# Optimization experiments

Hardware: AMD Instinct MI355X
Metric: run time of the kernel (lower is better)

## Reference

```python
import jax, jax.numpy as jnp
import numpy as np

DIM = 1024
EXP = 4           # expansion_factor
NUM_EXPERTS = 4
BATCH, SEQ = 4, 4096


def setup_inputs() -> dict:
    key = jax.random.key(0)
    ks = jax.random.split(key, 6)
    x = jax.random.normal(ks[0], (BATCH, SEQ, DIM), dtype=jnp.float32)
    token_mask = jax.random.randint(ks[1], (BATCH, SEQ), 0, NUM_EXPERTS, dtype=jnp.int32)
    hid = DIM * EXP
    s1 = 1.0 / np.sqrt(DIM)
    s2 = 1.0 / np.sqrt(hid)
    # nn.Linear layout: weight [out_features, in_features]
    w1 = jax.random.uniform(ks[2], (hid, DIM), minval=-s1, maxval=s1, dtype=jnp.float32)
    b1 = jax.random.uniform(ks[3], (hid,), minval=-s1, maxval=s1, dtype=jnp.float32)
    w2 = jax.random.uniform(ks[4], (DIM, hid), minval=-s2, maxval=s2, dtype=jnp.float32)
    b2 = jax.random.uniform(ks[5], (DIM,), minval=-s2, maxval=s2, dtype=jnp.float32)
    return {"x": x, "w1": w1, "b1": b1, "w2": w2, "b2": b2, "token_mask": token_mask}


def _nested_ffn(x, w1, b1, w2, b2, token_mask):
    dim = x.shape[-1]            # in_features of proj1
    out_dim = w2.shape[0]        # out_features of proj2 (== dim)
    # Expert m uses the first D_m = width >> (E-1-m) features (matryoshka nesting).
    # Expand (proj1): truncating input features to D_m and doing a full GEMM is
    # exactly equivalent to zeroing features >= D_m, so we mask then do one GEMM.
    d_in = dim >> (NUM_EXPERTS - 1 - token_mask)             # [B,S]
    in_mask = jnp.arange(dim) < d_in[..., None]              # [B,S,dim]
    h = jnp.einsum('bsd,fd->bsf', jnp.where(in_mask, x, jnp.zeros((), x.dtype)), w1) + b1
    h = jax.nn.gelu(h, approximate=False)                    # torch nn.GELU() default = erf
    # Contract (proj2): expert m produces only the first D_m outputs (incl. bias),
    # padded with zeros -> compute full GEMM then mask outputs.
    d_out = out_dim >> (NUM_EXPERTS - 1 - token_mask)        # [B,S]
    out_mask = jnp.arange(out_dim) < d_out[..., None]        # [B,S,out_dim]
    y = jnp.einsum('bsf,df->bsd', h, w2) + b2
    return jnp.where(out_mask, y, jnp.zeros((), y.dtype))


def reference(x, w1, b1, w2, b2, token_mask):
    return _nested_ffn(x, w1, b1, w2, b2, token_mask)
```

## Files before the change

kernel.cpp:

```cpp
#include <hip/hip_runtime.h>
#include <hip/hip_bf16.h>


typedef __bf16 bf16x8 __attribute__((ext_vector_type(8)));
typedef float f32x4 __attribute__((ext_vector_type(4)));

#define M_TOK   16384
#define DIM     1024
#define HID     4096

#define META_TK    40
#define META_BLK   64
#define META_MAP   256
#define META_RT    2560

__device__ inline unsigned int pk_bf16(float a, float b) {
  unsigned int r;
  asm("v_cvt_pk_bf16_f32 %0, %1, %2" : "=v"(r) : "v"(a), "v"(b));
  return r;
}

__device__ inline float gelu_f(float v) {
  float v2 = v * v;
  float w = v * fmaf(0.10294324f, v2, 2.30220830f);
  float e = __builtin_amdgcn_exp2f(-w);
  return v * __builtin_amdgcn_rcpf(1.0f + e);
}

__device__ inline void async_copy16(const void* g, void* s) {
  __builtin_amdgcn_global_load_lds(
      (const __attribute__((address_space(1))) unsigned int*)g,
      (__attribute__((address_space(3))) unsigned int*)s,
      16, 0, 0);
}

template<int ROWS, int LDK>
__device__ inline void stage_tile(const unsigned short* __restrict__ g,
                                  int row0, int k0, char* lds) {
  const char* gbase = (const char*)g;
  int tid = threadIdx.x;
#pragma unroll
  for (int i = 0; i < ROWS / 32; ++i) {
    int q = i * 256 + tid;
    int r = q >> 3;
    int c = q & 7;
    int gc = c ^ (r & 7);
    const void* gp = gbase + ((size_t)(row0 + r) * LDK + (size_t)k0 + gc * 8) * 2;
    async_copy16(gp, lds + (size_t)q * 16);
  }
}

__global__ __launch_bounds__(1024) void sortw_kernel(
    const int* __restrict__ tm,
    const float* __restrict__ w1,
    const float* __restrict__ w2,
    int* __restrict__ meta,
    unsigned short* __restrict__ w1b,
    unsigned short* __restrict__ w2b) {
  int tid = threadIdx.x;
  if (blockIdx.x != 0) {
    size_t i = (size_t)(blockIdx.x - 1) * 4096 + tid * 4;
    const float* src;
    unsigned short* dst;
    if (i < (size_t)HID * DIM) { src = w1; dst = w1b; }
    else { src = w2 - (size_t)HID * DIM; dst = w2b - (size_t)HID * DIM; }
    float4 v = *(const float4*)(src + i);
    uint2 o;
    o.x = pk_bf16(v.x, v.y);
    o.y = pk_bf16(v.z, v.w);
    *(uint2*)(dst + i) = o;
    return;
  }

  __shared__ unsigned short rt[16384];
  __shared__ unsigned int w01[16], w23[16];
  __shared__ int sbase[4];
  __shared__ int cb[128];
  int lane = tid & 63, wv = tid >> 6;

  int c0 = 0, c1 = 0, c2 = 0, c3 = 0;
  unsigned int epack = 0;
  int4 tv[4];
#pragma unroll
  for (int j = 0; j < 4; ++j)
    tv[j] = *(const int4*)(tm + tid * 16 + j * 4);
#pragma unroll
  for (int j = 0; j < 4; ++j) {
    int e;
    e = tv[j].x; epack |= (unsigned)e << (2 * (4 * j + 0)); c0 += (e == 0); c1 += (e == 1); c2 += (e == 2); c3 += (e == 3);
    e = tv[j].y; epack |= (unsigned)e << (2 * (4 * j + 1)); c0 += (e == 0); c1 += (e == 1); c2 += (e == 2); c3 += (e == 3);
    e = tv[j].z; epack |= (unsigned)e << (2 * (4 * j + 2)); c0 += (e == 0); c1 += (e == 1); c2 += (e == 2); c3 += (e == 3);
    e = tv[j].w; epack |= (unsigned)e << (2 * (4 * j + 3)); c0 += (e == 0); c1 += (e == 1); c2 += (e == 2); c3 += (e == 3);
  }
  unsigned int p01 = (unsigned)c0 | ((unsigned)c1 << 16);
  unsigned int p23 = (unsigned)c2 | ((unsigned)c3 << 16);
  unsigned int i01 = p01, i23 = p23;
#pragma unroll
  for (int s = 1; s < 64; s <<= 1) {
    unsigned int t0 = __shfl_up(i01, s, 64);
    unsigned int t1 = __shfl_up(i23, s, 64);
    if (lane >= s) { i01 += t0; i23 += t1; }
  }
  if (lane == 63) { w01[wv] = i01; w23[wv] = i23; }
  unsigned int e01 = i01 - p01, e23 = i23 - p23;
  __syncthreads();
  if (tid < 16) {
    unsigned int a = w01[tid], b = w23[tid];
    unsigned int ia = a, ib = b;
#pragma unroll
    for (int s = 1; s < 16; s <<= 1) {
      unsigned int t0 = __shfl_up(ia, s, 64);
      unsigned int t1 = __shfl_up(ib, s, 64);
      if (tid >= s) { ia += t0; ib += t1; }
    }
    w01[tid] = ia - a;
    w23[tid] = ib - b;
    if (tid == 15) {
      int t0 = (int)(ia & 0xFFFF), t1 = (int)(ia >> 16), t2 = (int)(ib & 0xFFFF);
      sbase[0] = 0; sbase[1] = t0; sbase[2] = t0 + t1; sbase[3] = t0 + t1 + t2;
    }
  }
  __syncthreads();
  int off0 = sbase[0] + (int)((w01[wv] & 0xFFFF) + (e01 & 0xFFFF));
  int off1 = sbase[1] + (int)((w01[wv] >> 16) + (e01 >> 16));
  int off2 = sbase[2] + (int)((w23[wv] & 0xFFFF) + (e23 & 0xFFFF));
  int off3 = sbase[3] + (int)((w23[wv] >> 16) + (e23 >> 16));
#pragma unroll
  for (int j = 0; j < 16; ++j) {
    int e = (epack >> (2 * j)) & 3;
    int t = tid * 16 + j;
    int pos = (e == 0) ? off0++ : (e == 1) ? off1++ : (e == 2) ? off2++ : off3++;
    rt[pos] = (unsigned short)(t | (e << 14));
  }
  __syncthreads();

  if (tid < 128) {
    int last = tid * 128 + 127;
    int e = (last >= sbase[1]) + (last >= sbase[2]) + (last >= sbase[3]);
    cb[tid] = 1 << e;
    meta[META_BLK + tid] = 128 << e;
  }
  __syncthreads();
  if (tid < 8) {
    int k = tid;
    int* map = meta + META_MAP + k * 128;
    int Tk = 0;
    for (int j = 0; j < 16; ++j) Tk += cb[k + 8 * j];
    meta[META_TK + k] = Tk;
    int pos = 0, zpos = Tk;
    for (int j = 0; j < 16; ++j) {
      int s = k + 8 * j;
      int n = cb[s];
      for (int c = 0; c < n; ++c) map[pos++] = s * 8 + c;
      for (int c = n; c < 8; ++c) map[zpos++] = s * 8 + c;
    }
  }
  int* rowtok = meta + META_RT;
#pragma unroll
  for (int j = 0; j < 16; ++j)
    rowtok[j * 1024 + tid] = (int)rt[j * 1024 + tid];
}

__global__ void prepx_kernel(const float* __restrict__ x,
                             const int* __restrict__ meta,
                             unsigned short* __restrict__ xb) {
  int b = blockIdx.x;
  int tid = threadIdx.x;
  int mt = meta[META_RT + b];
  int t = mt & 0x3FFF;
  int din = 128 << (mt >> 14);
  int kb = meta[META_BLK + (b >> 7)];
  int d = tid * 4;
  if (d < kb) {
    uint2 o; o.x = 0; o.y = 0;
    if (d < din) {
      float4 v = *(const float4*)(x + (size_t)t * DIM + d);
      o.x = pk_bf16(v.x, v.y);
      o.y = pk_bf16(v.z, v.w);
    }
    *(uint2*)(xb + (size_t)b * DIM + d) = o;
  }
}

__global__ __launch_bounds__(256) void gemm1_kernel(
    const unsigned short* __restrict__ A,
    const unsigned short* __restrict__ B,
    const float* __restrict__ bias,
    const int* __restrict__ meta,
    unsigned short* __restrict__ H)
{
  constexpr int K = DIM, N = HID;
  __shared__ char smem[32768];
  char* As = smem;
  char* Bs = smem + 16384;
  int tid = threadIdx.x;
  int lane = tid & 63, quad = lane >> 4, l15 = lane & 15;
  int wave = tid >> 6, wm = wave & 1, wn = wave >> 1;
  int rowblk = 127 - (blockIdx.x >> 5);
  int row0 = rowblk * 128, col0 = (blockIdx.x & 31) * 128;
  int kmax = meta[META_BLK + rowblk];

  int chb = (quad ^ (l15 & 7)) << 4;

  f32x4 acc[4][4] = {};

  for (int k0 = 0; k0 < kmax; k0 += 64) {
    __syncthreads();
    stage_tile<128, K>(A, row0, k0, As);
    stage_tile<128, K>(B, col0, k0, Bs);
    __syncthreads();
#pragma unroll
    for (int kk = 0; kk < 2; ++kk) {
      int xo = chb ^ (kk << 6);
      bf16x8 af[4], bg[4];
#pragma unroll
      for (int mt = 0; mt < 4; ++mt)
        af[mt] = *(const bf16x8*)(As + (wm * 64 + mt * 16 + l15) * 128 + xo);
#pragma unroll
      for (int nt = 0; nt < 4; ++nt)
        bg[nt] = *(const bf16x8*)(Bs + (wn * 64 + nt * 16 + l15) * 128 + xo);
#pragma unroll
      for (int mt = 0; mt < 4; ++mt)
#pragma unroll
        for (int nt = 0; nt < 4; ++nt)
          acc[mt][nt] = __builtin_amdgcn_mfma_f32_16x16x32_bf16(
              bg[nt], af[mt], acc[mt][nt], 0, 0, 0);
    }
  }

  int t_base = row0 + wm * 64;
  int f_base = col0 + wn * 64;
#pragma unroll
  for (int nt = 0; nt < 4; ++nt) {
    int f0 = f_base + nt * 16 + quad * 4;
    float4 bv = *(const float4*)(bias + f0);
#pragma unroll
    for (int mt = 0; mt < 4; ++mt) {
      int t = t_base + mt * 16 + l15;
      float v0 = gelu_f(acc[mt][nt][0] + bv.x);
      float v1 = gelu_f(acc[mt][nt][1] + bv.y);
      float v2 = gelu_f(acc[mt][nt][2] + bv.z);
      float v3 = gelu_f(acc[mt][nt][3] + bv.w);
      uint2 p;
      p.x = pk_bf16(v0, v1);
      p.y = pk_bf16(v2, v3);
      *(uint2*)(H + (size_t)t * N + f0) = p;
    }
  }
}

__global__ __launch_bounds__(256) void gemm2_kernel(
    const unsigned short* __restrict__ A,
    const unsigned short* __restrict__ B,
    const float* __restrict__ bias,
    const int* __restrict__ meta,
    float* __restrict__ out)
{
  constexpr int K = HID, N = DIM;
  int Bk = blockIdx.x & 7, ord = blockIdx.x >> 3;
  int Tk = meta[META_TK + Bk];
  int mp = meta[META_MAP + Bk * 128 + ord];
  int row0 = (mp >> 3) * 128, col0 = (mp & 7) * 128;
  const int* rowtok = meta + META_RT;
  int tid = threadIdx.x;

  if (ord >= Tk) {
    float4 z = make_float4(0.f, 0.f, 0.f, 0.f);
#pragma unroll
    for (int i = 0; i < 16; ++i) {
      int idx = i * 256 + tid;
      int r = idx >> 5;
      int col = (idx & 31) * 4;
      int t = rowtok[row0 + r] & 0x3FFF;
      *(float4*)(out + (size_t)t * N + col0 + col) = z;
    }
    return;
  }

  __shared__ char smem[32768];
  char* As = smem;
  char* Bs = smem + 16384;
  int lane = tid & 63, quad = lane >> 4, l15 = lane & 15;
  int wave = tid >> 6, wm = wave & 1, wn = wave >> 1;
  int chb = (quad ^ (l15 & 7)) << 4;

  f32x4 acc[4][4] = {};

  for (int k0 = 0; k0 < K; k0 += 64) {
    __syncthreads();
    stage_tile<128, K>(A, row0, k0, As);
    stage_tile<128, K>(B, col0, k0, Bs);
    __syncthreads();
#pragma unroll
    for (int kk = 0; kk < 2; ++kk) {
      int xo = chb ^ (kk << 6);
      bf16x8 af[4], bg[4];
#pragma unroll
      for (int mt = 0; mt < 4; ++mt)
        af[mt] = *(const bf16x8*)(As + (wm * 64 + mt * 16 + l15) * 128 + xo);
#pragma unroll
      for (int nt = 0; nt < 4; ++nt)
        bg[nt] = *(const bf16x8*)(Bs + (wn * 64 + nt * 16 + l15) * 128 + xo);
#pragma unroll
      for (int mt = 0; mt < 4; ++mt)
#pragma unroll
        for (int nt = 0; nt < 4; ++nt)
          acc[mt][nt] = __builtin_amdgcn_mfma_f32_16x16x32_bf16(
              bg[nt], af[mt], acc[mt][nt], 0, 0, 0);
    }
  }

  int p_base = row0 + wm * 64;
  int d_base = col0 + wn * 64;
  float4 bv[4];
#pragma unroll
  for (int nt = 0; nt < 4; ++nt)
    bv[nt] = *(const float4*)(bias + d_base + nt * 16 + quad * 4);
#pragma unroll
  for (int mt = 0; mt < 4; ++mt) {
    int m2 = rowtok[p_base + mt * 16 + l15];
    int t = m2 & 0x3FFF;
    int dout = 128 << (m2 >> 14);
#pragma unroll
    for (int nt = 0; nt < 4; ++nt) {
      int d0 = d_base + nt * 16 + quad * 4;
      bool ok = d0 < dout;
      float4 o;
      o.x = ok ? acc[mt][nt][0] + bv[nt].x : 0.0f;
      o.y = ok ? acc[mt][nt][1] + bv[nt].y : 0.0f;
      o.z = ok ? acc[mt][nt][2] + bv[nt].z : 0.0f;
      o.w = ok ? acc[mt][nt][3] + bv[nt].w : 0.0f;
      *(float4*)(out + (size_t)t * N + d0) = o;
    }
  }
}

extern "C" void kernel_launch(void* const* d_in, const int* in_sizes, int n_in,
                              void* d_out, int out_size, void* d_ws, size_t ws_size,
                              hipStream_t stream) {
  const float* x  = (const float*)d_in[0];
  const float* w1 = (const float*)d_in[1];
  const float* b1 = (const float*)d_in[2];
  const float* w2 = (const float*)d_in[3];
  const float* b2 = (const float*)d_in[4];
  const int*   tm = (const int*)d_in[5];
  float* out = (float*)d_out;

  char* ws = (char*)d_ws;
  int* meta = (int*)ws;
  unsigned short* xb  = (unsigned short*)(ws + 131072);
  unsigned short* w1b = (unsigned short*)(ws + 33685504);
  unsigned short* w2b = (unsigned short*)(ws + 42074112);
  unsigned short* hb  = (unsigned short*)(ws + 50462720);

  sortw_kernel<<<2049, 1024, 0, stream>>>(tm, w1, w2, meta, w1b, w2b);
  prepx_kernel<<<M_TOK, 256, 0, stream>>>(x, meta, xb);
  gemm1_kernel<<<4096, 256, 0, stream>>>(xb, w1b, b1, meta, hb);
  gemm2_kernel<<<1024, 256, 0, stream>>>(hb, w2b, b2, meta, out);
}
```

Baseline: 324.9 us.

## Double-buffer LDS tiles in both GEMM kernels to overlap loads with MFMA

Both GEMM kernels now use two 32KB LDS buffers. The next k-tile is staged into the alternate buffer while MFMAs consume the current one, and the loop uses one barrier per iteration instead of two. The aim is to hide global-to-LDS latency behind compute. The cost is that LDS per block doubles to 64KB, which reduces how many blocks can be resident per CU.

```diff
diff --git a/kernel.cpp b/kernel.cpp
--- a/kernel.cpp
+++ b/kernel.cpp
@@ -190,9 +190,7 @@
     unsigned short* __restrict__ H)
 {
   constexpr int K = DIM, N = HID;
-  __shared__ char smem[32768];
-  char* As = smem;
-  char* Bs = smem + 16384;
+  __shared__ char smem[65536];
   int tid = threadIdx.x;
   int lane = tid & 63, quad = lane >> 4, l15 = lane & 15;
   int wave = tid >> 6, wm = wave & 1, wn = wave >> 1;
@@ -204,11 +202,21 @@
 
   f32x4 acc[4][4] = {};
 
-  for (int k0 = 0; k0 < kmax; k0 += 64) {
-    __syncthreads();
-    stage_tile<128, K>(A, row0, k0, As);
-    stage_tile<128, K>(B, col0, k0, Bs);
-    __syncthreads();
+  stage_tile<128, K>(A, row0, 0, smem);
+  stage_tile<128, K>(B, col0, 0, smem + 16384);
+  __syncthreads();
+
+  int nt = kmax >> 6;
+  for (int t = 0; t < nt; ++t) {
+    char* buf = smem + ((t & 1) << 15);
+    if (t + 1 < nt) {
+      char* nbuf = smem + (((t + 1) & 1) << 15);
+      int kn = (t + 1) << 6;
+      stage_tile<128, K>(A, row0, kn, nbuf);
+      stage_tile<128, K>(B, col0, kn, nbuf + 16384);
+    }
+    char* As = buf;
+    char* Bs = buf + 16384;
 #pragma unroll
     for (int kk = 0; kk < 2; ++kk) {
       int xo = chb ^ (kk << 6);
@@ -217,30 +225,31 @@
       for (int mt = 0; mt < 4; ++mt)
         af[mt] = *(const bf16x8*)(As + (wm * 64 + mt * 16 + l15) * 128 + xo);
 #pragma unroll
-      for (int nt = 0; nt < 4; ++nt)
-        bg[nt] = *(const bf16x8*)(Bs + (wn * 64 + nt * 16 + l15) * 128 + xo);
+      for (int nt2 = 0; nt2 < 4; ++nt2)
+        bg[nt2] = *(const bf16x8*)(Bs + (wn * 64 + nt2 * 16 + l15) * 128 + xo);
 #pragma unroll
       for (int mt = 0; mt < 4; ++mt)
 #pragma unroll
-        for (int nt = 0; nt < 4; ++nt)
-          acc[mt][nt] = __builtin_amdgcn_mfma_f32_16x16x32_bf16(
-              bg[nt], af[mt], acc[mt][nt], 0, 0, 0);
-    }
+        for (int nt2 = 0; nt2 < 4; ++nt2)
+          acc[mt][nt2] = __builtin_amdgcn_mfma_f32_16x16x32_bf16(
+              bg[nt2], af[mt], acc[mt][nt2], 0, 0, 0);
+    }
+    __syncthreads();
   }
 
   int t_base = row0 + wm * 64;
   int f_base = col0 + wn * 64;
 #pragma unroll
-  for (int nt = 0; nt < 4; ++nt) {
-    int f0 = f_base + nt * 16 + quad * 4;
+  for (int nt2 = 0; nt2 < 4; ++nt2) {
+    int f0 = f_base + nt2 * 16 + quad * 4;
     float4 bv = *(const float4*)(bias + f0);
 #pragma unroll
     for (int mt = 0; mt < 4; ++mt) {
       int t = t_base + mt * 16 + l15;
-      float v0 = gelu_f(acc[mt][nt][0] + bv.x);
-      float v1 = gelu_f(acc[mt][nt][1] + bv.y);
-      float v2 = gelu_f(acc[mt][nt][2] + bv.z);
-      float v3 = gelu_f(acc[mt][nt][3] + bv.w);
+      float v0 = gelu_f(acc[mt][nt2][0] + bv.x);
+      float v1 = gelu_f(acc[mt][nt2][1] + bv.y);
+      float v2 = gelu_f(acc[mt][nt2][2] + bv.z);
+      float v3 = gelu_f(acc[mt][nt2][3] + bv.w);
       uint2 p;
       p.x = pk_bf16(v0, v1);
       p.y = pk_bf16(v2, v3);
@@ -277,20 +286,28 @@
     return;
   }
 
-  __shared__ char smem[32768];
-  char* As = smem;
-  char* Bs = smem + 16384;
+  __shared__ char smem[65536];
   int lane = tid & 63, quad = lane >> 4, l15 = lane & 15;
   int wave = tid >> 6, wm = wave & 1, wn = wave >> 1;
   int chb = (quad ^ (l15 & 7)) << 4;
 
   f32x4 acc[4][4] = {};
 
-  for (int k0 = 0; k0 < K; k0 += 64) {
-    __syncthreads();
-    stage_tile<128, K>(A, row0, k0, As);
-    stage_tile<128, K>(B, col0, k0, Bs);
-    __syncthreads();
+  stage_tile<128, K>(A, row0, 0, smem);
+  stage_tile<128, K>(B, col0, 0, smem + 16384);
+  __syncthreads();
+
+  constexpr int NT = K >> 6;
+  for (int t = 0; t < NT; ++t) {
+    char* buf = smem + ((t & 1) << 15);
+    if (t + 1 < NT) {
+      char* nbuf = smem + (((t + 1) & 1) << 15);
+      int kn = (t + 1) << 6;
+      stage_tile<128, K>(A, row0, kn, nbuf);
+      stage_tile<128, K>(B, col0, kn, nbuf + 16384);
+    }
+    char* As = buf;
+    char* Bs = buf + 16384;
 #pragma unroll
     for (int kk = 0; kk < 2; ++kk) {
       int xo = chb ^ (kk << 6);
@@ -299,37 +316,38 @@
       for (int mt = 0; mt < 4; ++mt)
         af[mt] = *(const bf16x8*)(As + (wm * 64 + mt * 16 + l15) * 128 + xo);
 #pragma unroll
-      for (int nt = 0; nt < 4; ++nt)
-        bg[nt] = *(const bf16x8*)(Bs + (wn * 64 + nt * 16 + l15) * 128 + xo);
+      for (int nt2 = 0; nt2 < 4; ++nt2)
+        bg[nt2] = *(const bf16x8*)(Bs + (wn * 64 + nt2 * 16 + l15) * 128 + xo);
 #pragma unroll
       for (int mt = 0; mt < 4; ++mt)
 #pragma unroll
-        for (int nt = 0; nt < 4; ++nt)
-          acc[mt][nt] = __builtin_amdgcn_mfma_f32_16x16x32_bf16(
-              bg[nt], af[mt], acc[mt][nt], 0, 0, 0);
-    }
+        for (int nt2 = 0; nt2 < 4; ++nt2)
+          acc[mt][nt2] = __builtin_amdgcn_mfma_f32_16x16x32_bf16(
+              bg[nt2], af[mt], acc[mt][nt2], 0, 0, 0);
+    }
+    __syncthreads();
   }
 
   int p_base = row0 + wm * 64;
   int d_base = col0 + wn * 64;
   float4 bv[4];
 #pragma unroll
-  for (int nt = 0; nt < 4; ++nt)
-    bv[nt] = *(const float4*)(bias + d_base + nt * 16 + quad * 4);
+  for (int nt2 = 0; nt2 < 4; ++nt2)
+    bv[nt2] = *(const float4*)(bias + d_base + nt2 * 16 + quad * 4);
 #pragma unroll
   for (int mt = 0; mt < 4; ++mt) {
     int m2 = rowtok[p_base + mt * 16 + l15];
     int t = m2 & 0x3FFF;
     int dout = 128 << (m2 >> 14);
 #pragma unroll
-    for (int nt = 0; nt < 4; ++nt) {
-      int d0 = d_base + nt * 16 + quad * 4;
+    for (int nt2 = 0; nt2 < 4; ++nt2) {
+      int d0 = d_base + nt2 * 16 + quad * 4;
       bool ok = d0 < dout;
       float4 o;
-      o.x = ok ? acc[mt][nt][0] + bv[nt].x : 0.0f;
-      o.y = ok ? acc[mt][nt][1] + bv[nt].y : 0.0f;
-      o.z = ok ? acc[mt][nt][2] + bv[nt].z : 0.0f;
-      o.w = ok ? acc[mt][nt][3] + bv[nt].w : 0.0f;
+      o.x = ok ? acc[mt][nt2][0] + bv[nt2].x : 0.0f;
+      o.y = ok ? acc[mt][nt2][1] + bv[nt2].y : 0.0f;
+      o.z = ok ? acc[mt][nt2][2] + bv[nt2].z : 0.0f;
+      o.w = ok ? acc[mt][nt2][3] + bv[nt2].w : 0.0f;
       *(float4*)(out + (size_t)t * N + d0) = o;
     }
   }
```

Result: faster. 314.3 us (-3.3%).
